# Optimization experiments

Measured on AMD Instinct MI355X. Metric: run time of the kernel, lower is better.

## Reference

```python
import jax, jax.numpy as jnp
import numpy as np

N_NODES = 50000
N_EDGES = 800000
N_GRAPHS = 64
IN_C, HID_C, OUT_C, N_CLS = 128, 128, 64, 2


def _linear_params(key, fan_in, fan_out):
    kw, kb = jax.random.split(key)
    s = 1.0 / np.sqrt(fan_in)
    W = jax.random.uniform(kw, (fan_out, fan_in), jnp.float32, -s, s)
    b = jax.random.uniform(kb, (fan_out,), jnp.float32, -s, s)
    return W, b


def setup_inputs() -> dict:
    key = jax.random.key(0)
    ks = jax.random.split(key, 12)
    x = jax.random.normal(ks[0], (N_NODES, IN_C), jnp.float32)
    edge_index = jax.random.randint(ks[1], (2, N_EDGES), 0, N_NODES, jnp.int32)
    batch = jnp.sort(jax.random.randint(ks[2], (N_NODES,), 0, N_GRAPHS, jnp.int32))
    inp = {"x": x, "edge_index": edge_index, "batch": batch}
    # conv1 params (in=128 -> hid=128): key, query, value, skip linears
    for i, nm in enumerate(["k", "q", "v", "s"]):
        W, b = _linear_params(ks[3 + i], IN_C, HID_C)
        inp[f"w1{nm}"], inp[f"b1{nm}"] = W, b
    # conv2 params (hid=128 -> 64)
    for i, nm in enumerate(["k", "q", "v", "s"]):
        W, b = _linear_params(ks[7 + i], HID_C, OUT_C)
        inp[f"w2{nm}"], inp[f"b2{nm}"] = W, b
    wfc, bfc = _linear_params(ks[11], OUT_C, N_CLS)
    inp["wfc"], inp["bfc"] = wfc, bfc
    return inp


def _res_gated_conv(x, src, dst, Wk, bk, Wq, bq, Wv, bv, Ws, bs):
    # PyG ResGatedGraphConv: eta_ij = sigmoid(k_i + q_j), out_i = skip(x_i) + sum_j eta_ij * v_j
    k = x @ Wk.T + bk  # [N, C_out] (target transform)
    q = x @ Wq.T + bq  # [N, C_out] (source transform)
    v = x @ Wv.T + bv  # [N, C_out]
    eta = jax.nn.sigmoid(k[dst] + q[src])          # [E, C_out]
    msg = eta * v[src]                              # [E, C_out]
    agg = jax.ops.segment_sum(msg, dst, num_segments=x.shape[0])
    return agg + (x @ Ws.T + bs)


def reference(x, edge_index, batch,
              w1k, b1k, w1q, b1q, w1v, b1v, w1s, b1s,
              w2k, b2k, w2q, b2q, w2v, b2v, w2s, b2s,
              wfc, bfc):
    src, dst = edge_index[0], edge_index[1]
    h = jax.nn.relu(_res_gated_conv(x, src, dst, w1k, b1k, w1q, b1q, w1v, b1v, w1s, b1s))
    h = jax.nn.relu(_res_gated_conv(h, src, dst, w2k, b2k, w2q, b2q, w2v, b2v, w2s, b2s))
    # global_mean_pool over graphs
    sums = jax.ops.segment_sum(h, batch, num_segments=N_GRAPHS)            # [G, 64]
    cnts = jax.ops.segment_sum(jnp.ones((h.shape[0],), h.dtype), batch, num_segments=N_GRAPHS)
    pooled = sums / jnp.maximum(cnts, 1.0)[:, None]
    # dropout is identity in eval mode
    return pooled @ wfc.T + bfc  # [G, num_classes]
```

## Files before the change

### kernel.cpp

```cpp
#include <hip/hip_runtime.h>
#include <hip/hip_bf16.h>
#include <math.h>

#define N_NODES 50000
#define N_EDGES 800000
#define N_GRAPHS 64
#define SCAN_BLOCKS 196

typedef __attribute__((ext_vector_type(8))) short short8v;
typedef __attribute__((ext_vector_type(4))) float float4v;

static constexpr size_t OFF_K1   = 0;
static constexpr size_t OFF_S1   = 12800000;
static constexpr size_t OFF_QV1  = 25600000;
static constexpr size_t OFF_H1B  = 51200000;
static constexpr size_t OFF_XB   = 64000000;
static constexpr size_t OFF_K2   = 0;
static constexpr size_t OFF_S2   = 6400000;
static constexpr size_t OFF_QV2  = 12800000;
static constexpr size_t OFF_H2   = 25600000;
static constexpr size_t OFF_ESRC = 76800000;
static constexpr size_t OFF_OFFS = 80000000;
static constexpr size_t OFF_CURS = 80200064;
static constexpr size_t OFF_BSUM = 80400064;
static constexpr size_t OFF_BBAS = 80400848;
static constexpr size_t OFF_BP1  = 80401664;
static constexpr size_t OFF_BC1  = 80532736;
static constexpr size_t OFF_BP2  = 80534784;
static constexpr size_t OFF_BC2  = 80600320;
static constexpr size_t OFF_SG   = 80601344;
static constexpr size_t OFF_EG   = 80601600;
static constexpr size_t OFF_PL   = 80601856;

#define NLOG2E 1.44269504f

__device__ inline unsigned short f2bf(float f) {
    __hip_bfloat16 h = __float2bfloat16(f);
    union { __hip_bfloat16 h; unsigned short u; } cv;
    cv.h = h;
    return cv.u;
}
__device__ inline float fast_exp2(float x) { float r; asm("v_exp_f32 %0, %1" : "=v"(r) : "v"(x)); return r; }
__device__ inline float fast_rcp (float x) { float r; asm("v_rcp_f32 %0, %1" : "=v"(r) : "v"(x)); return r; }
__device__ inline float u2f(unsigned int u) { union { unsigned int i; float f; } w; w.i = u; return w.f; }

__device__ inline void gacc2(uint2 qv, float kx, float ky, float& ax, float& ay) {
    float q0 = u2f(qv.x << 16), v0 = u2f(qv.x & 0xffff0000u);
    float q1 = u2f(qv.y << 16), v1 = u2f(qv.y & 0xffff0000u);
    ax += v0 * fast_rcp(1.f + fast_exp2(kx + q0));
    ay += v1 * fast_rcp(1.f + fast_exp2(ky + q1));
}
__device__ inline void gacc1(unsigned int qv, float k, float& a) {
    float q = u2f(qv << 16), v = u2f(qv & 0xffff0000u);
    a += v * fast_rcp(1.f + fast_exp2(k + q));
}

__global__ void cast_kernel(const float* __restrict__ x, unsigned short* __restrict__ xb) {
    int id = blockIdx.x * 256 + threadIdx.x;
    float4 v0 = *(const float4*)&x[(size_t)id * 8];
    float4 v1 = *(const float4*)&x[(size_t)id * 8 + 4];
    short8v o;
    o[0] = (short)f2bf(v0.x); o[1] = (short)f2bf(v0.y);
    o[2] = (short)f2bf(v0.z); o[3] = (short)f2bf(v0.w);
    o[4] = (short)f2bf(v1.x); o[5] = (short)f2bf(v1.y);
    o[6] = (short)f2bf(v1.z); o[7] = (short)f2bf(v1.w);
    *(short8v*)(xb + (size_t)id * 8) = o;
}

__global__ void prep1_kernel(const float* __restrict__ wk, const float* __restrict__ bk,
                             const float* __restrict__ wq, const float* __restrict__ bq,
                             const float* __restrict__ wv, const float* __restrict__ bv,
                             const float* __restrict__ ws, const float* __restrict__ bs,
                             unsigned short* __restrict__ Bp, float* __restrict__ bcat) {
    int id = blockIdx.x * 256 + threadIdx.x;
    if (id < 8192) {
        int l = id & 63, ks = (id >> 6) & 3, ct = id >> 8;
        int c = ct * 16 + (l & 15);
        int g = c >> 7, n = c & 127;
        const float* W = (g == 0) ? wk : (g == 1) ? wq : (g == 2) ? wv : ws;
        int kb = ks * 32 + ((l >> 4) << 3);
        short8v o;
#pragma unroll
        for (int j = 0; j < 8; ++j) o[j] = (short)f2bf(W[n * 128 + kb + j]);
        *(short8v*)(Bp + (size_t)id * 8) = o;
    }
    if (id < 512) {
        int g = id >> 7, n = id & 127;
        const float* B = (g == 0) ? bk : (g == 1) ? bq : (g == 2) ? bv : bs;
        bcat[id] = B[n];
    }
}

__global__ void prep2_kernel(const float* __restrict__ wk, const float* __restrict__ bk,
                             const float* __restrict__ wq, const float* __restrict__ bq,
                             const float* __restrict__ wv, const float* __restrict__ bv,
                             const float* __restrict__ ws, const float* __restrict__ bs,
                             unsigned short* __restrict__ Bp, float* __restrict__ bcat) {
    int id = blockIdx.x * 256 + threadIdx.x;
    if (id < 4096) {
        int l = id & 63, ks = (id >> 6) & 3, ct = id >> 8;
        int c = ct * 16 + (l & 15);
        int g = c >> 6, n = c & 63;
        const float* W = (g == 0) ? wk : (g == 1) ? wq : (g == 2) ? wv : ws;
        int kb = ks * 32 + ((l >> 4) << 3);
        short8v o;
#pragma unroll
        for (int j = 0; j < 8; ++j) o[j] = (short)f2bf(W[n * 128 + kb + j]);
        *(short8v*)(Bp + (size_t)id * 8) = o;
    }
    if (id < 256) {
        int g = id >> 6, n = id & 63;
        const float* B = (g == 0) ? bk : (g == 1) ? bq : (g == 2) ? bv : bs;
        bcat[id] = B[n];
    }
}

__global__ void hist_kernel(const int* __restrict__ dst, int* __restrict__ hist) {
    int e = blockIdx.x * 256 + threadIdx.x;
    if (e < N_EDGES) atomicAdd(&hist[dst[e]], 1);
}

__global__ void bsum_kernel(const int* __restrict__ hist, int* __restrict__ bsum) {
    int t = threadIdx.x;
    int idx = blockIdx.x * 256 + t;
    __shared__ int sh[256];
    sh[t] = (idx < N_NODES) ? hist[idx] : 0;
    __syncthreads();
    for (int d = 128; d > 0; d >>= 1) {
        if (t < d) sh[t] += sh[t + d];
        __syncthreads();
    }
    if (t == 0) bsum[blockIdx.x] = sh[0];
}

__global__ void bscan_kernel(const int* __restrict__ bsum, int* __restrict__ bbase) {
    int t = threadIdx.x;
    __shared__ int sh[256];
    sh[t] = (t < SCAN_BLOCKS) ? bsum[t] : 0;
    __syncthreads();
    for (int d = 1; d < 256; d <<= 1) {
        int v = (t >= d) ? sh[t - d] : 0;
        __syncthreads();
        sh[t] += v;
        __syncthreads();
    }
    if (t < SCAN_BLOCKS) bbase[t] = (t == 0) ? 0 : sh[t - 1];
}

__global__ void offs_kernel(const int* __restrict__ hist, const int* __restrict__ bbase,
                            int* __restrict__ offs, int* __restrict__ cursor) {
    int t = threadIdx.x;
    int idx = blockIdx.x * 256 + t;
    int v = (idx < N_NODES) ? hist[idx] : 0;
    __shared__ int sh[256];
    sh[t] = v;
    __syncthreads();
    for (int d = 1; d < 256; d <<= 1) {
        int u = (t >= d) ? sh[t - d] : 0;
        __syncthreads();
        sh[t] += u;
        __syncthreads();
    }
    if (idx < N_NODES) {
        int o = bbase[blockIdx.x] + sh[t] - v;
        offs[idx] = o;
        cursor[idx] = o;
    }
    if (idx == 0) offs[N_NODES] = N_EDGES;
}

__global__ void fill_kernel(const int* __restrict__ src, const int* __restrict__ dst,
                            int* __restrict__ cursor, int* __restrict__ esrc) {
    int e = blockIdx.x * 256 + threadIdx.x;
    if (e < N_EDGES) {
        int d = dst[e];
        int pos = atomicAdd(&cursor[d], 1);
        esrc[pos] = src[e];
    }
}

template <int LAYER>
__global__ __launch_bounds__(256) void gemm_mfma(const unsigned short* __restrict__ Ab,
                                                 const unsigned short* __restrict__ Bp,
                                                 const float* __restrict__ bias,
                                                 unsigned short* __restrict__ Kout,
                                                 unsigned short* __restrict__ Sout,
                                                 unsigned short* __restrict__ QVout,
                                                 int M) {
    __shared__ __align__(16) unsigned char As[32768];
    const int tid = threadIdx.x;
    const int w = tid >> 6, l = tid & 63;
    const int lx = l & 15, lg = l >> 4;
    const int row0 = blockIdx.x * 128;
    const int colb = blockIdx.y * 128;

#pragma unroll
    for (int i = 0; i < 8; ++i) {
        int id = i * 256 + tid;
        int r = id >> 4, c = id & 15;
        int gr = row0 + r;
        short8v v;
#pragma unroll
        for (int j = 0; j < 8; ++j) v[j] = 0;
        if (gr < M) v = *(const short8v*)(Ab + (size_t)gr * 128 + c * 8);
        *(short8v*)(As + r * 256 + ((c ^ (r & 7)) << 4)) = v;
    }
    __syncthreads();

    float4v acc[2][8];
#pragma unroll
    for (int m = 0; m < 2; ++m)
#pragma unroll
        for (int n = 0; n < 8; ++n)
#pragma unroll
            for (int q = 0; q < 4; ++q) acc[m][n][q] = 0.f;

    const int ct0 = blockIdx.y * 8;
#pragma unroll
    for (int ks = 0; ks < 4; ++ks) {
        short8v a[2];
#pragma unroll
        for (int m = 0; m < 2; ++m) {
            int rl = 32 * w + 16 * m + lx;
            int cc = ks * 4 + lg;
            a[m] = *(const short8v*)(As + rl * 256 + ((cc ^ (rl & 7)) << 4));
        }
#pragma unroll
        for (int n = 0; n < 8; ++n) {
            short8v b = *(const short8v*)(Bp + (size_t)(((ct0 + n) * 4 + ks) * 64 + l) * 8);
            acc[0][n] = __builtin_amdgcn_mfma_f32_16x16x32_bf16(a[0], b, acc[0][n], 0, 0, 0);
            acc[1][n] = __builtin_amdgcn_mfma_f32_16x16x32_bf16(a[1], b, acc[1][n], 0, 0, 0);
        }
    }

    float bb[8];
#pragma unroll
    for (int n = 0; n < 8; ++n) bb[n] = bias[colb + 16 * n + lx];

    const int rbase = row0 + 32 * w + 4 * lg;
#pragma unroll
    for (int m = 0; m < 2; ++m) {
#pragma unroll
        for (int reg = 0; reg < 4; ++reg) {
            int r = rbase + 16 * m + reg;
            if (r >= M) continue;
#pragma unroll
            for (int n = 0; n < 8; ++n) {
                float val = acc[m][n][reg] + bb[n];
                int c = 16 * n + lx;
                if (LAYER == 1) {
                    if (blockIdx.y == 0)      Kout[(size_t)r * 128 + c] = f2bf(-NLOG2E * val);
                    else if (blockIdx.y == 1) QVout[(size_t)r * 256 + 2 * c]     = f2bf(-NLOG2E * val);
                    else if (blockIdx.y == 2) QVout[(size_t)r * 256 + 2 * c + 1] = f2bf(val);
                    else                      Sout[(size_t)r * 128 + c] = f2bf(val);
                } else {
                    if (blockIdx.y == 0) {
                        if (c < 64) Kout[(size_t)r * 64 + c] = f2bf(-NLOG2E * val);
                        else        QVout[(size_t)r * 128 + 2 * (c - 64)] = f2bf(-NLOG2E * val);
                    } else {
                        if (c < 64) QVout[(size_t)r * 128 + 2 * c + 1] = f2bf(val);
                        else        Sout[(size_t)r * 64 + (c - 64)] = f2bf(val);
                    }
                }
            }
        }
    }
}

__global__ __launch_bounds__(256) void edge1_kernel(const unsigned short* __restrict__ K1b,
                                                    const unsigned short* __restrict__ S1b,
                                                    const unsigned int* __restrict__ QV,
                                                    const int* __restrict__ offs,
                                                    const int* __restrict__ esrc,
                                                    unsigned short* __restrict__ H1B) {
    int node = __builtin_amdgcn_readfirstlane(blockIdx.x * 4 + (threadIdx.x >> 6));
    int lane = threadIdx.x & 63;
    unsigned int kr = *(const unsigned int*)(K1b + (size_t)node * 128 + lane * 2);
    unsigned int sr = *(const unsigned int*)(S1b + (size_t)node * 128 + lane * 2);
    float kx = u2f(kr << 16), ky = u2f(kr & 0xffff0000u);
    float sx = u2f(sr << 16), sy = u2f(sr & 0xffff0000u);
    float ax0 = 0.f, ay0 = 0.f, ax1 = 0.f, ay1 = 0.f;
    float ax2 = 0.f, ay2 = 0.f, ax3 = 0.f, ay3 = 0.f;
    int e0 = offs[node], e1 = offs[node + 1];
    int j = e0;
    for (; j + 4 <= e1; j += 4) {
        int s0 = esrc[j], s1 = esrc[j + 1], s2 = esrc[j + 2], s3 = esrc[j + 3];
        uint2 a = *(const uint2*)(QV + (size_t)s0 * 128 + lane * 2);
        uint2 b = *(const uint2*)(QV + (size_t)s1 * 128 + lane * 2);
        uint2 c = *(const uint2*)(QV + (size_t)s2 * 128 + lane * 2);
        uint2 d = *(const uint2*)(QV + (size_t)s3 * 128 + lane * 2);
        gacc2(a, kx, ky, ax0, ay0);
        gacc2(b, kx, ky, ax1, ay1);
        gacc2(c, kx, ky, ax2, ay2);
        gacc2(d, kx, ky, ax3, ay3);
    }
    for (; j < e1; ++j) {
        uint2 a = *(const uint2*)(QV + (size_t)esrc[j] * 128 + lane * 2);
        gacc2(a, kx, ky, ax0, ay0);
    }
    float rx = sx + (ax0 + ax1) + (ax2 + ax3);
    float ry = sy + (ay0 + ay1) + (ay2 + ay3);
    ushort2 o;
    o.x = f2bf(rx > 0.f ? rx : 0.f);
    o.y = f2bf(ry > 0.f ? ry : 0.f);
    *(ushort2*)(H1B + (size_t)node * 128 + lane * 2) = o;
}

__global__ __launch_bounds__(256) void edge2_kernel(const unsigned short* __restrict__ K2b,
                                                    const unsigned short* __restrict__ S2b,
                                                    const unsigned int* __restrict__ QV,
                                                    const int* __restrict__ offs,
                                                    const int* __restrict__ esrc,
                                                    float* __restrict__ H2) {
    int node = __builtin_amdgcn_readfirstlane(blockIdx.x * 4 + (threadIdx.x >> 6));
    int lane = threadIdx.x & 63;
    float k1 = u2f(((unsigned int)K2b[(size_t)node * 64 + lane]) << 16);
    float s1 = u2f(((unsigned int)S2b[(size_t)node * 64 + lane]) << 16);
    float a0 = 0.f, a1 = 0.f, a2 = 0.f, a3 = 0.f;
    int e0 = offs[node], e1 = offs[node + 1];
    int j = e0;
    for (; j + 4 <= e1; j += 4) {
        unsigned int qa = QV[(size_t)esrc[j] * 64 + lane];
        unsigned int qb = QV[(size_t)esrc[j + 1] * 64 + lane];
        unsigned int qc = QV[(size_t)esrc[j + 2] * 64 + lane];
        unsigned int qd = QV[(size_t)esrc[j + 3] * 64 + lane];
        gacc1(qa, k1, a0);
        gacc1(qb, k1, a1);
        gacc1(qc, k1, a2);
        gacc1(qd, k1, a3);
    }
    for (; j < e1; ++j) gacc1(QV[(size_t)esrc[j] * 64 + lane], k1, a0);
    float r = s1 + (a0 + a1) + (a2 + a3);
    H2[(size_t)node * 64 + lane] = r > 0.f ? r : 0.f;
}

__global__ void bounds_kernel(const int* __restrict__ batch, int* __restrict__ sg,
                              int* __restrict__ eg) {
    int n = blockIdx.x * 256 + threadIdx.x;
    if (n >= N_NODES) return;
    int b = batch[n];
    if (n == 0) {
        sg[b] = 0;
    } else {
        int p = batch[n - 1];
        if (p != b) { sg[b] = n; eg[p] = n - 1; }
    }
    if (n == N_NODES - 1) eg[b] = N_NODES - 1;
}

__global__ void pool_kernel(const float* __restrict__ H2, const int* __restrict__ sg,
                            const int* __restrict__ eg, float* __restrict__ pooled) {
    int g = blockIdx.x;
    int s = sg[g], e = eg[g];
    int ch = threadIdx.x & 63, sub = threadIdx.x >> 6;
    float acc = 0.f;
    for (int n = s + sub; n <= e; n += 4) acc += H2[(size_t)n * 64 + ch];
    __shared__ float red[4][64];
    red[sub][ch] = acc;
    __syncthreads();
    if (sub == 0) {
        float v = red[0][ch] + red[1][ch] + red[2][ch] + red[3][ch];
        int cnt = e - s + 1;
        if (cnt < 1) cnt = 1;
        pooled[g * 64 + ch] = v / (float)cnt;
    }
}

__global__ void fc_kernel(const float* __restrict__ pooled, const float* __restrict__ wfc,
                          const float* __restrict__ bfc, float* __restrict__ out) {
    int t = threadIdx.x;
    int g = t >> 1, c = t & 1;
    float s = bfc[c];
#pragma unroll
    for (int i = 0; i < 64; ++i) s += pooled[g * 64 + i] * wfc[c * 64 + i];
    out[g * 2 + c] = s;
}

extern "C" void kernel_launch(void* const* d_in, const int* in_sizes, int n_in,
                              void* d_out, int out_size, void* d_ws, size_t ws_size,
                              hipStream_t stream) {
    (void)in_sizes; (void)n_in; (void)out_size; (void)ws_size;
    const float* x    = (const float*)d_in[0];
    const int*   ei   = (const int*)d_in[1];
    const int*   batch= (const int*)d_in[2];
    const float* w1k = (const float*)d_in[3];  const float* b1k = (const float*)d_in[4];
    const float* w1q = (const float*)d_in[5];  const float* b1q = (const float*)d_in[6];
    const float* w1v = (const float*)d_in[7];  const float* b1v = (const float*)d_in[8];
    const float* w1s = (const float*)d_in[9];  const float* b1s = (const float*)d_in[10];
    const float* w2k = (const float*)d_in[11]; const float* b2k = (const float*)d_in[12];
    const float* w2q = (const float*)d_in[13]; const float* b2q = (const float*)d_in[14];
    const float* w2v = (const float*)d_in[15]; const float* b2v = (const float*)d_in[16];
    const float* w2s = (const float*)d_in[17]; const float* b2s = (const float*)d_in[18];
    const float* wfc = (const float*)d_in[19]; const float* bfc = (const float*)d_in[20];
    float* out = (float*)d_out;

    char* ws = (char*)d_ws;
    unsigned short* K1  = (unsigned short*)(ws + OFF_K1);
    unsigned short* S1  = (unsigned short*)(ws + OFF_S1);
    unsigned short* QV1 = (unsigned short*)(ws + OFF_QV1);
    unsigned short* H1B = (unsigned short*)(ws + OFF_H1B);
    unsigned short* XB  = (unsigned short*)(ws + OFF_XB);
    unsigned short* K2  = (unsigned short*)(ws + OFF_K2);
    unsigned short* S2  = (unsigned short*)(ws + OFF_S2);
    unsigned short* QV2 = (unsigned short*)(ws + OFF_QV2);
    float* H2   = (float*)(ws + OFF_H2);
    int*   esrc = (int*)(ws + OFF_ESRC);
    int*   offs = (int*)(ws + OFF_OFFS);
    int*   curs = (int*)(ws + OFF_CURS);
    int*   bsum = (int*)(ws + OFF_BSUM);
    int*   bbas = (int*)(ws + OFF_BBAS);
    unsigned short* BP1 = (unsigned short*)(ws + OFF_BP1);
    float* bc1  = (float*)(ws + OFF_BC1);
    unsigned short* BP2 = (unsigned short*)(ws + OFF_BP2);
    float* bc2  = (float*)(ws + OFF_BC2);
    int*   sg   = (int*)(ws + OFF_SG);
    int*   eg   = (int*)(ws + OFF_EG);
    float* pl   = (float*)(ws + OFF_PL);

    const int* src = ei;
    const int* dst = ei + N_EDGES;

    prep1_kernel<<<32, 256, 0, stream>>>(w1k, b1k, w1q, b1q, w1v, b1v, w1s, b1s, BP1, bc1);
    prep2_kernel<<<16, 256, 0, stream>>>(w2k, b2k, w2q, b2q, w2v, b2v, w2s, b2s, BP2, bc2);
    cast_kernel<<<3125, 256, 0, stream>>>(x, XB);

    hipMemsetAsync(curs, 0, N_NODES * sizeof(int), stream);
    hist_kernel<<<(N_EDGES + 255) / 256, 256, 0, stream>>>(dst, curs);
    bsum_kernel<<<SCAN_BLOCKS, 256, 0, stream>>>(curs, bsum);
    bscan_kernel<<<1, 256, 0, stream>>>(bsum, bbas);
    offs_kernel<<<SCAN_BLOCKS, 256, 0, stream>>>(curs, bbas, offs, curs);
    fill_kernel<<<(N_EDGES + 255) / 256, 256, 0, stream>>>(src, dst, curs, esrc);

    gemm_mfma<1><<<dim3(391, 4), 256, 0, stream>>>(XB, BP1, bc1, K1, S1, QV1, N_NODES);
    edge1_kernel<<<12500, 256, 0, stream>>>(K1, S1, (const unsigned int*)QV1, offs, esrc, H1B);

    gemm_mfma<2><<<dim3(391, 2), 256, 0, stream>>>(H1B, BP2, bc2, K2, S2, QV2, N_NODES);
    edge2_kernel<<<12500, 256, 0, stream>>>(K2, S2, (const unsigned int*)QV2, offs, esrc, H2);

    hipMemsetAsync(sg, 0x7f, N_GRAPHS * sizeof(int), stream);
    hipMemsetAsync(eg, 0x80, N_GRAPHS * sizeof(int), stream);
    bounds_kernel<<<(N_NODES + 255) / 256, 256, 0, stream>>>(batch, sg, eg);
    pool_kernel<<<N_GRAPHS, 256, 0, stream>>>(H2, sg, eg, pl);
    fc_kernel<<<1, 128, 0, stream>>>(pl, wfc, bfc, out);
}
```

Before: 336.9 us.

## Stage GEMM outputs through LDS and widen edge gathers to 16-byte loads

```diff
diff --git a/kernel.cpp b/kernel.cpp
--- a/kernel.cpp
+++ b/kernel.cpp
@@ -44,15 +44,15 @@
 __device__ inline float fast_rcp (float x) { float r; asm("v_rcp_f32 %0, %1" : "=v"(r) : "v"(x)); return r; }
 __device__ inline float u2f(unsigned int u) { union { unsigned int i; float f; } w; w.i = u; return w.f; }
 
-__device__ inline void gacc2(uint2 qv, float kx, float ky, float& ax, float& ay) {
+__device__ inline void gacc4(uint4 qv, float k0, float k1, float k2, float k3, float* a) {
     float q0 = u2f(qv.x << 16), v0 = u2f(qv.x & 0xffff0000u);
     float q1 = u2f(qv.y << 16), v1 = u2f(qv.y & 0xffff0000u);
-    ax += v0 * fast_rcp(1.f + fast_exp2(kx + q0));
-    ay += v1 * fast_rcp(1.f + fast_exp2(ky + q1));
-}
-__device__ inline void gacc1(unsigned int qv, float k, float& a) {
-    float q = u2f(qv << 16), v = u2f(qv & 0xffff0000u);
-    a += v * fast_rcp(1.f + fast_exp2(k + q));
+    float q2 = u2f(qv.z << 16), v2 = u2f(qv.z & 0xffff0000u);
+    float q3 = u2f(qv.w << 16), v3 = u2f(qv.w & 0xffff0000u);
+    a[0] += v0 * fast_rcp(1.f + fast_exp2(k0 + q0));
+    a[1] += v1 * fast_rcp(1.f + fast_exp2(k1 + q1));
+    a[2] += v2 * fast_rcp(1.f + fast_exp2(k2 + q2));
+    a[3] += v3 * fast_rcp(1.f + fast_exp2(k3 + q3));
 }
 
 __global__ void cast_kernel(const float* __restrict__ x, unsigned short* __restrict__ xb) {
@@ -179,20 +179,19 @@
     }
 }
 
-template <int LAYER>
-__global__ __launch_bounds__(256) void gemm_mfma(const unsigned short* __restrict__ Ab,
-                                                 const unsigned short* __restrict__ Bp,
-                                                 const float* __restrict__ bias,
-                                                 unsigned short* __restrict__ Kout,
-                                                 unsigned short* __restrict__ Sout,
-                                                 unsigned short* __restrict__ QVout,
-                                                 int M) {
+__global__ __launch_bounds__(256) void gemm1_kernel(const unsigned short* __restrict__ Ab,
+                                                    const unsigned short* __restrict__ Bp,
+                                                    const float* __restrict__ bias,
+                                                    unsigned short* __restrict__ Kout,
+                                                    unsigned short* __restrict__ Sout,
+                                                    unsigned short* __restrict__ QVout,
+                                                    int M) {
     __shared__ __align__(16) unsigned char As[32768];
     const int tid = threadIdx.x;
     const int w = tid >> 6, l = tid & 63;
     const int lx = l & 15, lg = l >> 4;
     const int row0 = blockIdx.x * 128;
-    const int colb = blockIdx.y * 128;
+    const bool isKS = (blockIdx.y == 0);
 
 #pragma unroll
     for (int i = 0; i < 8; ++i) {
@@ -207,15 +206,16 @@
     }
     __syncthreads();
 
-    float4v acc[2][8];
+    float4v acc[2][16];
 #pragma unroll
     for (int m = 0; m < 2; ++m)
 #pragma unroll
-        for (int n = 0; n < 8; ++n)
+        for (int n = 0; n < 16; ++n)
 #pragma unroll
             for (int q = 0; q < 4; ++q) acc[m][n][q] = 0.f;
 
-    const int ct0 = blockIdx.y * 8;
+    const int ctA = isKS ? 0 : 8;
+    const int ctB = isKS ? 24 : 16;
 #pragma unroll
     for (int ks = 0; ks < 4; ++ks) {
         short8v a[2];
@@ -226,43 +226,206 @@
             a[m] = *(const short8v*)(As + rl * 256 + ((cc ^ (rl & 7)) << 4));
         }
 #pragma unroll
-        for (int n = 0; n < 8; ++n) {
-            short8v b = *(const short8v*)(Bp + (size_t)(((ct0 + n) * 4 + ks) * 64 + l) * 8);
+        for (int n = 0; n < 16; ++n) {
+            int ct = (n < 8) ? (ctA + n) : (ctB + n - 8);
+            short8v b = *(const short8v*)(Bp + (size_t)((ct * 4 + ks) * 64 + l) * 8);
             acc[0][n] = __builtin_amdgcn_mfma_f32_16x16x32_bf16(a[0], b, acc[0][n], 0, 0, 0);
             acc[1][n] = __builtin_amdgcn_mfma_f32_16x16x32_bf16(a[1], b, acc[1][n], 0, 0, 0);
         }
     }
 
-    float bb[8];
-#pragma unroll
-    for (int n = 0; n < 8; ++n) bb[n] = bias[colb + 16 * n + lx];
-
-    const int rbase = row0 + 32 * w + 4 * lg;
-#pragma unroll
-    for (int m = 0; m < 2; ++m) {
-#pragma unroll
-        for (int reg = 0; reg < 4; ++reg) {
-            int r = rbase + 16 * m + reg;
-            if (r >= M) continue;
-#pragma unroll
-            for (int n = 0; n < 8; ++n) {
-                float val = acc[m][n][reg] + bb[n];
-                int c = 16 * n + lx;
-                if (LAYER == 1) {
-                    if (blockIdx.y == 0)      Kout[(size_t)r * 128 + c] = f2bf(-NLOG2E * val);
-                    else if (blockIdx.y == 1) QVout[(size_t)r * 256 + 2 * c]     = f2bf(-NLOG2E * val);
-                    else if (blockIdx.y == 2) QVout[(size_t)r * 256 + 2 * c + 1] = f2bf(val);
-                    else                      Sout[(size_t)r * 128 + c] = f2bf(val);
-                } else {
-                    if (blockIdx.y == 0) {
-                        if (c < 64) Kout[(size_t)r * 64 + c] = f2bf(-NLOG2E * val);
-                        else        QVout[(size_t)r * 128 + 2 * (c - 64)] = f2bf(-NLOG2E * val);
-                    } else {
-                        if (c < 64) QVout[(size_t)r * 128 + 2 * c + 1] = f2bf(val);
-                        else        Sout[(size_t)r * 64 + (c - 64)] = f2bf(val);
+    const int colA0 = isKS ? 0 : 128;
+    const int colB0 = isKS ? 384 : 256;
+    float bbA[8], bbB[8];
+#pragma unroll
+    for (int n = 0; n < 8; ++n) {
+        bbA[n] = bias[colA0 + 16 * n + lx];
+        bbB[n] = bias[colB0 + 16 * n + lx];
+    }
+
+    const int rl0 = 32 * w + 4 * lg;
+    if (isKS) {
+        for (int plane = 0; plane < 2; ++plane) {
+            __syncthreads();
+#pragma unroll
+            for (int m = 0; m < 2; ++m)
+#pragma unroll
+                for (int reg = 0; reg < 4; ++reg) {
+                    int r = rl0 + 16 * m + reg;
+#pragma unroll
+                    for (int n = 0; n < 8; ++n) {
+                        float val = acc[m][plane * 8 + n][reg] + (plane ? bbB[n] : bbA[n]);
+                        if (plane == 0) val = -NLOG2E * val;
+                        int c = 16 * n + lx;
+                        int off = r * 256 + (((c >> 3) ^ (r & 7)) << 4) + ((c & 7) << 1);
+                        *(unsigned short*)(As + off) = f2bf(val);
                     }
                 }
+            __syncthreads();
+            unsigned short* Out = plane ? Sout : Kout;
+#pragma unroll
+            for (int i = 0; i < 8; ++i) {
+                int id = i * 256 + tid;
+                int row = id >> 4, k = id & 15;
+                int gr = row0 + row;
+                if (gr < M) {
+                    short8v v = *(const short8v*)(As + row * 256 + ((k ^ (row & 7)) << 4));
+                    *(short8v*)(Out + (size_t)gr * 128 + k * 8) = v;
+                }
             }
+        }
+    } else {
+        for (int h = 0; h < 2; ++h) {
+            __syncthreads();
+#pragma unroll
+            for (int m = 0; m < 2; ++m)
+#pragma unroll
+                for (int reg = 0; reg < 4; ++reg) {
+                    int r = rl0 + 16 * m + reg;
+                    if ((r >> 6) == h) {
+                        int rr = r & 63;
+#pragma unroll
+                        for (int n = 0; n < 8; ++n) {
+                            float qval = -NLOG2E * (acc[m][n][reg] + bbA[n]);
+                            float vval = acc[m][8 + n][reg] + bbB[n];
+                            int c = 16 * n + lx;
+                            int off = rr * 512 + (((c >> 2) ^ (rr & 7)) << 4) + ((c & 3) << 2);
+                            *(unsigned short*)(As + off)     = f2bf(qval);
+                            *(unsigned short*)(As + off + 2) = f2bf(vval);
+                        }
+                    }
+                }
+            __syncthreads();
+#pragma unroll
+            for (int i = 0; i < 8; ++i) {
+                int id = i * 256 + tid;
+                int row = id >> 5, k = id & 31;
+                int gr = row0 + h * 64 + row;
+                if (gr < M) {
+                    short8v v = *(const short8v*)(As + row * 512 + ((k ^ (row & 7)) << 4));
+                    *(short8v*)(QVout + (size_t)gr * 256 + k * 8) = v;
+                }
+            }
+        }
+    }
+}
+
+__global__ __launch_bounds__(256) void gemm2_kernel(const unsigned short* __restrict__ Ab,
+                                                    const unsigned short* __restrict__ Bp,
+                                                    const float* __restrict__ bias,
+                                                    unsigned short* __restrict__ Kout,
+                                                    unsigned short* __restrict__ Sout,
+                                                    unsigned short* __restrict__ QVout,
+                                                    int M) {
+    __shared__ __align__(16) unsigned char As[32768];
+    const int tid = threadIdx.x;
+    const int w = tid >> 6, l = tid & 63;
+    const int lx = l & 15, lg = l >> 4;
+    const int row0 = blockIdx.x * 128;
+
+#pragma unroll
+    for (int i = 0; i < 8; ++i) {
+        int id = i * 256 + tid;
+        int r = id >> 4, c = id & 15;
+        int gr = row0 + r;
+        short8v v;
+#pragma unroll
+        for (int j = 0; j < 8; ++j) v[j] = 0;
+        if (gr < M) v = *(const short8v*)(Ab + (size_t)gr * 128 + c * 8);
+        *(short8v*)(As + r * 256 + ((c ^ (r & 7)) << 4)) = v;
+    }
+    __syncthreads();
+
+    float4v acc[2][16];
+#pragma unroll
+    for (int m = 0; m < 2; ++m)
+#pragma unroll
+        for (int n = 0; n < 16; ++n)
+#pragma unroll
+            for (int q = 0; q < 4; ++q) acc[m][n][q] = 0.f;
+
+#pragma unroll
+    for (int ks = 0; ks < 4; ++ks) {
+        short8v a[2];
+#pragma unroll
+        for (int m = 0; m < 2; ++m) {
+            int rl = 32 * w + 16 * m + lx;
+            int cc = ks * 4 + lg;
+            a[m] = *(const short8v*)(As + rl * 256 + ((cc ^ (rl & 7)) << 4));
+        }
+#pragma unroll
+        for (int n = 0; n < 16; ++n) {
+            short8v b = *(const short8v*)(Bp + (size_t)((n * 4 + ks) * 64 + l) * 8);
+            acc[0][n] = __builtin_amdgcn_mfma_f32_16x16x32_bf16(a[0], b, acc[0][n], 0, 0, 0);
+            acc[1][n] = __builtin_amdgcn_mfma_f32_16x16x32_bf16(a[1], b, acc[1][n], 0, 0, 0);
+        }
+    }
+
+    float bbk[4], bbq[4], bbv[4], bbs[4];
+#pragma unroll
+    for (int n = 0; n < 4; ++n) {
+        bbk[n] = bias[16 * n + lx];
+        bbq[n] = bias[64 + 16 * n + lx];
+        bbv[n] = bias[128 + 16 * n + lx];
+        bbs[n] = bias[192 + 16 * n + lx];
+    }
+
+    const int rl0 = 32 * w + 4 * lg;
+    __syncthreads();
+#pragma unroll
+    for (int m = 0; m < 2; ++m)
+#pragma unroll
+        for (int reg = 0; reg < 4; ++reg) {
+            int r = rl0 + 16 * m + reg;
+#pragma unroll
+            for (int n = 0; n < 4; ++n) {
+                int c = 16 * n + lx;
+                int off = r * 128 + (((c >> 3) ^ (r & 7)) << 4) + ((c & 7) << 1);
+                float kv = -NLOG2E * (acc[m][n][reg] + bbk[n]);
+                float sv = acc[m][12 + n][reg] + bbs[n];
+                *(unsigned short*)(As + off)         = f2bf(kv);
+                *(unsigned short*)(As + 16384 + off) = f2bf(sv);
+            }
+        }
+    __syncthreads();
+#pragma unroll
+    for (int i = 0; i < 8; ++i) {
+        int id = i * 256 + tid;
+        int half = id >> 10;
+        int id2 = id & 1023;
+        int row = id2 >> 3, k = id2 & 7;
+        int gr = row0 + row;
+        if (gr < M) {
+            short8v v = *(const short8v*)(As + half * 16384 + row * 128 + ((k ^ (row & 7)) << 4));
+            unsigned short* Out = half ? Sout : Kout;
+            *(short8v*)(Out + (size_t)gr * 64 + k * 8) = v;
+        }
+    }
+    __syncthreads();
+#pragma unroll
+    for (int m = 0; m < 2; ++m)
+#pragma unroll
+        for (int reg = 0; reg < 4; ++reg) {
+            int r = rl0 + 16 * m + reg;
+#pragma unroll
+            for (int n = 0; n < 4; ++n) {
+                int c = 16 * n + lx;
+                int off = r * 256 + (((c >> 2) ^ (r & 7)) << 4) + ((c & 3) << 2);
+                float qv_ = -NLOG2E * (acc[m][4 + n][reg] + bbq[n]);
+                float vv  = acc[m][8 + n][reg] + bbv[n];
+                *(unsigned short*)(As + off)     = f2bf(qv_);
+                *(unsigned short*)(As + off + 2) = f2bf(vv);
+            }
+        }
+    __syncthreads();
+#pragma unroll
+    for (int i = 0; i < 8; ++i) {
+        int id = i * 256 + tid;
+        int row = id >> 4, k = id & 15;
+        int gr = row0 + row;
+        if (gr < M) {
+            short8v v = *(const short8v*)(As + row * 256 + ((k ^ (row & 7)) << 4));
+            *(short8v*)(QVout + (size_t)gr * 128 + k * 8) = v;
         }
     }
 }
@@ -275,35 +438,54 @@
                                                     unsigned short* __restrict__ H1B) {
     int node = __builtin_amdgcn_readfirstlane(blockIdx.x * 4 + (threadIdx.x >> 6));
     int lane = threadIdx.x & 63;
-    unsigned int kr = *(const unsigned int*)(K1b + (size_t)node * 128 + lane * 2);
-    unsigned int sr = *(const unsigned int*)(S1b + (size_t)node * 128 + lane * 2);
-    float kx = u2f(kr << 16), ky = u2f(kr & 0xffff0000u);
-    float sx = u2f(sr << 16), sy = u2f(sr & 0xffff0000u);
-    float ax0 = 0.f, ay0 = 0.f, ax1 = 0.f, ay1 = 0.f;
-    float ax2 = 0.f, ay2 = 0.f, ax3 = 0.f, ay3 = 0.f;
+    int half = lane >> 5, cl = lane & 31;
+    uint2 kk = *(const uint2*)(K1b + (size_t)node * 128 + cl * 4);
+    uint2 ss = *(const uint2*)(S1b + (size_t)node * 128 + cl * 4);
+    float k0 = u2f(kk.x << 16), k1 = u2f(kk.x & 0xffff0000u);
+    float k2 = u2f(kk.y << 16), k3 = u2f(kk.y & 0xffff0000u);
+    float a0[4] = {0.f, 0.f, 0.f, 0.f};
+    float a1[4] = {0.f, 0.f, 0.f, 0.f};
     int e0 = offs[node], e1 = offs[node + 1];
     int j = e0;
-    for (; j + 4 <= e1; j += 4) {
-        int s0 = esrc[j], s1 = esrc[j + 1], s2 = esrc[j + 2], s3 = esrc[j + 3];
-        uint2 a = *(const uint2*)(QV + (size_t)s0 * 128 + lane * 2);
-        uint2 b = *(const uint2*)(QV + (size_t)s1 * 128 + lane * 2);
-        uint2 c = *(const uint2*)(QV + (size_t)s2 * 128 + lane * 2);
-        uint2 d = *(const uint2*)(QV + (size_t)s3 * 128 + lane * 2);
-        gacc2(a, kx, ky, ax0, ay0);
-        gacc2(b, kx, ky, ax1, ay1);
-        gacc2(c, kx, ky, ax2, ay2);
-        gacc2(d, kx, ky, ax3, ay3);
-    }
-    for (; j < e1; ++j) {
-        uint2 a = *(const uint2*)(QV + (size_t)esrc[j] * 128 + lane * 2);
-        gacc2(a, kx, ky, ax0, ay0);
-    }
-    float rx = sx + (ax0 + ax1) + (ax2 + ax3);
-    float ry = sy + (ay0 + ay1) + (ay2 + ay3);
-    ushort2 o;
-    o.x = f2bf(rx > 0.f ? rx : 0.f);
-    o.y = f2bf(ry > 0.f ? ry : 0.f);
-    *(ushort2*)(H1B + (size_t)node * 128 + lane * 2) = o;
+    for (; j + 8 <= e1; j += 8) {
+        int s0 = esrc[j + 0 + half];
+        int s1 = esrc[j + 2 + half];
+        int s2 = esrc[j + 4 + half];
+        int s3 = esrc[j + 6 + half];
+        uint4 g0 = *(const uint4*)(QV + (size_t)s0 * 128 + cl * 4);
+        uint4 g1 = *(const uint4*)(QV + (size_t)s1 * 128 + cl * 4);
+        uint4 g2 = *(const uint4*)(QV + (size_t)s2 * 128 + cl * 4);
+        uint4 g3 = *(const uint4*)(QV + (size_t)s3 * 128 + cl * 4);
+        gacc4(g0, k0, k1, k2, k3, a0);
+        gacc4(g1, k0, k1, k2, k3, a1);
+        gacc4(g2, k0, k1, k2, k3, a0);
+        gacc4(g3, k0, k1, k2, k3, a1);
+    }
+    for (; j < e1; j += 2) {
+        int jj = j + half;
+        if (jj < e1) {
+            int s = esrc[jj];
+            uint4 g = *(const uint4*)(QV + (size_t)s * 128 + cl * 4);
+            gacc4(g, k0, k1, k2, k3, a0);
+        }
+    }
+    float t0 = a0[0] + a1[0], t1 = a0[1] + a1[1];
+    float t2 = a0[2] + a1[2], t3 = a0[3] + a1[3];
+    t0 += __shfl_xor(t0, 32);
+    t1 += __shfl_xor(t1, 32);
+    t2 += __shfl_xor(t2, 32);
+    t3 += __shfl_xor(t3, 32);
+    if (half == 0) {
+        float s0 = u2f(ss.x << 16), s1 = u2f(ss.x & 0xffff0000u);
+        float s2 = u2f(ss.y << 16), s3 = u2f(ss.y & 0xffff0000u);
+        float r0 = s0 + t0, r1 = s1 + t1, r2 = s2 + t2, r3 = s3 + t3;
+        ushort4 o;
+        o.x = f2bf(r0 > 0.f ? r0 : 0.f);
+        o.y = f2bf(r1 > 0.f ? r1 : 0.f);
+        o.z = f2bf(r2 > 0.f ? r2 : 0.f);
+        o.w = f2bf(r3 > 0.f ? r3 : 0.f);
+        *(ushort4*)(H1B + (size_t)node * 128 + cl * 4) = o;
+    }
 }
 
 __global__ __launch_bounds__(256) void edge2_kernel(const unsigned short* __restrict__ K2b,
@@ -314,24 +496,47 @@
                                                     float* __restrict__ H2) {
     int node = __builtin_amdgcn_readfirstlane(blockIdx.x * 4 + (threadIdx.x >> 6));
     int lane = threadIdx.x & 63;
-    float k1 = u2f(((unsigned int)K2b[(size_t)node * 64 + lane]) << 16);
-    float s1 = u2f(((unsigned int)S2b[(size_t)node * 64 + lane]) << 16);
-    float a0 = 0.f, a1 = 0.f, a2 = 0.f, a3 = 0.f;
+    int quart = lane >> 4, cl = lane & 15;
+    uint2 kk = *(const uint2*)(K2b + (size_t)node * 64 + cl * 4);
+    uint2 ss = *(const uint2*)(S2b + (size_t)node * 64 + cl * 4);
+    float k0 = u2f(kk.x << 16), k1 = u2f(kk.x & 0xffff0000u);
+    float k2 = u2f(kk.y << 16), k3 = u2f(kk.y & 0xffff0000u);
+    float a0[4] = {0.f, 0.f, 0.f, 0.f};
+    float a1[4] = {0.f, 0.f, 0.f, 0.f};
     int e0 = offs[node], e1 = offs[node + 1];
     int j = e0;
-    for (; j + 4 <= e1; j += 4) {
-        unsigned int qa = QV[(size_t)esrc[j] * 64 + lane];
-        unsigned int qb = QV[(size_t)esrc[j + 1] * 64 + lane];
-        unsigned int qc = QV[(size_t)esrc[j + 2] * 64 + lane];
-        unsigned int qd = QV[(size_t)esrc[j + 3] * 64 + lane];
-        gacc1(qa, k1, a0);
-        gacc1(qb, k1, a1);
-        gacc1(qc, k1, a2);
-        gacc1(qd, k1, a3);
-    }
-    for (; j < e1; ++j) gacc1(QV[(size_t)esrc[j] * 64 + lane], k1, a0);
-    float r = s1 + (a0 + a1) + (a2 + a3);
-    H2[(size_t)node * 64 + lane] = r > 0.f ? r : 0.f;
+    for (; j + 8 <= e1; j += 8) {
+        int s0 = esrc[j + quart];
+        int s1 = esrc[j + 4 + quart];
+        uint4 g0 = *(const uint4*)(QV + (size_t)s0 * 64 + cl * 4);
+        uint4 g1 = *(const uint4*)(QV + (size_t)s1 * 64 + cl * 4);
+        gacc4(g0, k0, k1, k2, k3, a0);
+        gacc4(g1, k0, k1, k2, k3, a1);
+    }
+    for (; j < e1; j += 4) {
+        int jj = j + quart;
+        if (jj < e1) {
+            int s = esrc[jj];
+            uint4 g = *(const uint4*)(QV + (size_t)s * 64 + cl * 4);
+            gacc4(g, k0, k1, k2, k3, a0);
+        }
+    }
+    float t0 = a0[0] + a1[0], t1 = a0[1] + a1[1];
+    float t2 = a0[2] + a1[2], t3 = a0[3] + a1[3];
+    t0 += __shfl_xor(t0, 16); t0 += __shfl_xor(t0, 32);
+    t1 += __shfl_xor(t1, 16); t1 += __shfl_xor(t1, 32);
+    t2 += __shfl_xor(t2, 16); t2 += __shfl_xor(t2, 32);
+    t3 += __shfl_xor(t3, 16); t3 += __shfl_xor(t3, 32);
+    if (quart == 0) {
+        float s0 = u2f(ss.x << 16), s1 = u2f(ss.x & 0xffff0000u);
+        float s2 = u2f(ss.y << 16), s3 = u2f(ss.y & 0xffff0000u);
+        float4 o;
+        o.x = fmaxf(s0 + t0, 0.f);
+        o.y = fmaxf(s1 + t1, 0.f);
+        o.z = fmaxf(s2 + t2, 0.f);
+        o.w = fmaxf(s3 + t3, 0.f);
+        *(float4*)(H2 + (size_t)node * 64 + cl * 4) = o;
+    }
 }
 
 __global__ void bounds_kernel(const int* __restrict__ batch, int* __restrict__ sg,
@@ -431,10 +636,10 @@
     offs_kernel<<<SCAN_BLOCKS, 256, 0, stream>>>(curs, bbas, offs, curs);
     fill_kernel<<<(N_EDGES + 255) / 256, 256, 0, stream>>>(src, dst, curs, esrc);
 
-    gemm_mfma<1><<<dim3(391, 4), 256, 0, stream>>>(XB, BP1, bc1, K1, S1, QV1, N_NODES);
+    gemm1_kernel<<<dim3(391, 2), 256, 0, stream>>>(XB, BP1, bc1, K1, S1, QV1, N_NODES);
     edge1_kernel<<<12500, 256, 0, stream>>>(K1, S1, (const unsigned int*)QV1, offs, esrc, H1B);
 
-    gemm_mfma<2><<<dim3(391, 2), 256, 0, stream>>>(H1B, BP2, bc2, K2, S2, QV2, N_NODES);
+    gemm2_kernel<<<391, 256, 0, stream>>>(H1B, BP2, bc2, K2, S2, QV2, N_NODES);
     edge2_kernel<<<12500, 256, 0, stream>>>(K2, S2, (const unsigned int*)QV2, offs, esrc, H2);
 
     hipMemsetAsync(sg, 0x7f, N_GRAPHS * sizeof(int), stream);
```

New measurement: 340.6 us. Within noise of the previous version (+1.1%).
